# Kernel optimization log

Measured on AMD Instinct MI355X. Metric: run time of the kernel, lower is better.

The kernel has to match this reference:

```python
import jax, jax.numpy as jnp
import numpy as np

D_MODEL = 1024


def setup_inputs() -> dict:
    key = jax.random.key(0)
    k1, k2, k3 = jax.random.split(key, 3)
    x = jax.random.normal(k1, (4, 2048, D_MODEL), dtype=jnp.float32)
    w_qkv = jax.random.normal(k2, (D_MODEL, 3 * D_MODEL), dtype=jnp.float32) * (D_MODEL ** -0.5)
    b_qkv = jnp.zeros((3 * D_MODEL,), dtype=jnp.float32)
    w_out = jax.random.normal(k3, (D_MODEL, D_MODEL), dtype=jnp.float32) * (D_MODEL ** -0.5)
    b_out = jnp.zeros((D_MODEL,), dtype=jnp.float32)
    return {"x": x, "w_qkv": w_qkv, "b_qkv": b_qkv, "w_out": w_out, "b_out": b_out}


def reference(x, w_qkv, b_qkv, w_out, b_out):
    # x: [B, S, D]
    d_model = x.shape[-1]
    scale = jnp.asarray(d_model, x.dtype) ** 0.5
    qkv = x @ w_qkv + b_qkv                      # [B, S, 3D]
    q, k, v = jnp.split(qkv, 3, axis=-1)          # each [B, S, D]
    scores = jnp.einsum('bsd,btd->bst', q, k) / scale  # [B, S, S]
    attn = jax.nn.softmax(scores, axis=-1)
    out = jnp.einsum('bst,btd->bsd', attn, v)     # [B, S, D]
    return out @ w_out + b_out
```

## Files before the change

### kernel.cpp

```cpp
#include <hip/hip_runtime.h>
#include <hip/hip_bf16.h>
#include <cstdint>

typedef __attribute__((ext_vector_type(8))) short bf16x8;
typedef __attribute__((ext_vector_type(4))) float f32x4;
using bf16 = __hip_bfloat16;

static __device__ __forceinline__ float tofloat(float x) { return x; }
static __device__ __forceinline__ float tofloat(bf16 x) { return __bfloat162float(x); }
static __device__ __forceinline__ void storeval(float* p, float v) { *p = v; }
static __device__ __forceinline__ void storeval(bf16* p, float v) { *p = __float2bfloat16(v); }

#define MFMA_BF16 __builtin_amdgcn_mfma_f32_16x16x32_bf16

template <int N>
static __device__ __forceinline__ void vm_wait() {
    if constexpr (N == 0) asm volatile("s_waitcnt vmcnt(0)" ::: "memory");
    else if constexpr (N == 6) asm volatile("s_waitcnt vmcnt(6)" ::: "memory");
    else if constexpr (N == 8) asm volatile("s_waitcnt vmcnt(8)" ::: "memory");
}
static __device__ __forceinline__ void lgkm0() {
    asm volatile("s_waitcnt lgkmcnt(0)" ::: "memory");
    __builtin_amdgcn_sched_barrier(0);
}
static __device__ __forceinline__ void bar() { __builtin_amdgcn_s_barrier(); }
static __device__ __forceinline__ void vmem_fence() { __builtin_amdgcn_sched_barrier(0x38F); }
static __device__ __forceinline__ void gl_lds(const bf16* src, char* dst) {
    __builtin_amdgcn_global_load_lds((const __attribute__((address_space(1))) unsigned int*)src,
                                     (__attribute__((address_space(3))) unsigned int*)dst, 16, 0, 0);
}

__global__ __launch_bounds__(256) void convert_f32_bf16(const float* __restrict__ in,
                                                        bf16* __restrict__ out, long n) {
    long i = ((long)blockIdx.x * blockDim.x + threadIdx.x) * 8;
    if (i >= n) return;
    float4 a = *(const float4*)(in + i);
    float4 b = *(const float4*)(in + i + 4);
    bf16 t[8];
    t[0] = __float2bfloat16(a.x); t[1] = __float2bfloat16(a.y);
    t[2] = __float2bfloat16(a.z); t[3] = __float2bfloat16(a.w);
    t[4] = __float2bfloat16(b.x); t[5] = __float2bfloat16(b.y);
    t[6] = __float2bfloat16(b.z); t[7] = __float2bfloat16(b.w);
    *(uint4*)(out + i) = *(const uint4*)t;
}

template <typename SrcT>
__global__ __launch_bounds__(256) void transpose_to_bf16(const SrcT* __restrict__ src, long srcStride,
                                                         long srcBatch, bf16* __restrict__ dst,
                                                         long dstStride, long dstBatch) {
    __shared__ float tile[32][33];
    const SrcT* s = src + (long)blockIdx.z * srcBatch;
    bf16* d = dst + (long)blockIdx.z * dstBatch;
    long r0 = (long)blockIdx.y * 32, c0 = (long)blockIdx.x * 32;
    for (int i = threadIdx.y; i < 32; i += 8)
        tile[i][threadIdx.x] = tofloat(s[(r0 + i) * srcStride + c0 + threadIdx.x]);
    __syncthreads();
    for (int i = threadIdx.y; i < 32; i += 8)
        d[(c0 + i) * dstStride + r0 + threadIdx.x] = __float2bfloat16(tile[threadIdx.x][i]);
}

template <typename OutT, bool BIAS, int BM>
__global__ __launch_bounds__(512, 2) void gemm8p(
    const bf16* __restrict__ Ag, long lda, long batchA,
    const bf16* __restrict__ Bg, long ldb, long batchB,
    OutT* __restrict__ Cg, long ldc, long batchC,
    const float* __restrict__ bias, int K, float alpha, int nx, int ny) {
    constexpr int MR = BM / 32;
    constexpr int LA = BM / 128;
    constexpr int PA = BM * 64;
    constexpr int PB = 16384;
    constexpr int WV = 4 + 2 * LA;
    extern __shared__ __align__(16) char smem[];

    const int tid = threadIdx.x;
    const int wave = tid >> 6, lane = tid & 63, l16 = lane & 15, lhi = lane >> 4;
    const int wm = wave >> 2, wn = wave & 3;

    const int nwg = gridDim.x;
    const int l = (blockIdx.x & 7) * (nwg >> 3) + (blockIdx.x >> 3);
    const int pt = nx * ny;
    const int z = l / pt, rr = l % pt;
    const long mtile = (long)(rr / nx) * BM;
    const long ntile = (long)(rr % nx) * 256;

    const bf16* A = Ag + (long)z * batchA;
    const bf16* B = Bg + (long)z * batchB;
    OutT* C = Cg + (long)z * batchC;

    const int rp0 = tid >> 3;
    const int g8 = ((tid & 7) ^ ((tid >> 4) & 7)) * 8;
    const bf16* pA = A + (mtile + rp0) * lda + g8;
    const bf16* pB = B + (ntile + rp0) * ldb + g8;
    const int wb = wave * 1024;

    auto stageB = [&](int par, int t) {
        const bf16* s0 = pB + (long)t * 64;
        char* d0 = smem + 4 * PA + par * PB + wb;
        gl_lds(s0, d0);
        gl_lds(s0 + 64 * ldb, d0 + 8192);
        const bf16* s1 = s0 + 128 * ldb;
        char* d1 = smem + 4 * PA + 2 * PB + par * PB + wb;
        gl_lds(s1, d1);
        gl_lds(s1 + 64 * ldb, d1 + 8192);
    };
    auto stageA = [&](int par, int t) {
        const bf16* s0 = pA + (long)t * 64;
        char* d0 = smem + par * PA + wb;
        gl_lds(s0, d0);
        if constexpr (LA == 2) gl_lds(s0 + 64 * lda, d0 + 8192);
        const bf16* s1 = s0 + (long)(BM / 2) * lda;
        char* d1 = smem + 2 * PA + par * PA + wb;
        gl_lds(s1, d1);
        if constexpr (LA == 2) gl_lds(s1 + 64 * lda, d1 + 8192);
    };

    const int swz = (l16 >> 1) & 7;
    const int cb0 = (lhi ^ swz) * 16;
    const int cb1 = ((4 + lhi) ^ swz) * 16;
    const char* aBase = smem + wm * 2 * PA + l16 * 128;
    const char* bBase = smem + 4 * PA + (wn >> 1) * 2 * PB + ((wn & 1) * 64 + l16) * 128;

    bf16x8 aq[MR], bq[8];
    f32x4 acc[MR][4];
#pragma unroll
    for (int m = 0; m < MR; ++m)
#pragma unroll
        for (int n = 0; n < 4; ++n) acc[m][n] = f32x4{0.f, 0.f, 0.f, 0.f};

#define LDA_(par, h)                                                           \
    do {                                                                       \
        const char* p_ = aBase + (par) * PA + (h) * (PA / 2);                  \
        _Pragma("unroll")                                                      \
        for (int m_ = 0; m_ < MR / 2; ++m_) {                                  \
            aq[2 * m_]     = *(const bf16x8*)(p_ + m_ * 2048 + cb0);           \
            aq[2 * m_ + 1] = *(const bf16x8*)(p_ + m_ * 2048 + cb1);           \
        }                                                                      \
    } while (0)

#define LDB_(par, nlo)                                                         \
    do {                                                                       \
        const char* p_ = bBase + (par) * PB + (nlo) * 2048;                    \
        bq[(nlo) * 2 + 0] = *(const bf16x8*)(p_ + cb0);                        \
        bq[(nlo) * 2 + 1] = *(const bf16x8*)(p_ + cb1);                        \
        bq[(nlo) * 2 + 2] = *(const bf16x8*)(p_ + 2048 + cb0);                 \
        bq[(nlo) * 2 + 3] = *(const bf16x8*)(p_ + 2048 + cb1);                 \
    } while (0)

#define QUAD_(h, nlo)                                                          \
    do {                                                                       \
        __builtin_amdgcn_s_setprio(1);                                         \
        _Pragma("unroll")                                                      \
        for (int m_ = 0; m_ < MR / 2; ++m_) {                                  \
            acc[(h) * (MR / 2) + m_][(nlo) + 0] =                              \
                MFMA_BF16(aq[2 * m_], bq[(nlo) * 2 + 0], acc[(h) * (MR / 2) + m_][(nlo) + 0], 0, 0, 0); \
            acc[(h) * (MR / 2) + m_][(nlo) + 1] =                              \
                MFMA_BF16(aq[2 * m_], bq[(nlo) * 2 + 2], acc[(h) * (MR / 2) + m_][(nlo) + 1], 0, 0, 0); \
        }                                                                      \
        _Pragma("unroll")                                                      \
        for (int m_ = 0; m_ < MR / 2; ++m_) {                                  \
            acc[(h) * (MR / 2) + m_][(nlo) + 0] =                              \
                MFMA_BF16(aq[2 * m_ + 1], bq[(nlo) * 2 + 1], acc[(h) * (MR / 2) + m_][(nlo) + 0], 0, 0, 0); \
            acc[(h) * (MR / 2) + m_][(nlo) + 1] =                              \
                MFMA_BF16(aq[2 * m_ + 1], bq[(nlo) * 2 + 3], acc[(h) * (MR / 2) + m_][(nlo) + 1], 0, 0, 0); \
        }                                                                      \
        __builtin_amdgcn_s_setprio(0);                                         \
    } while (0)

#define KTILE(par, tstage, MODE)                                               \
    do {                                                                       \
                                                                       \
        LDA_(par, 0); LDB_(par, 0);                                            \
        bar(); lgkm0();                                                        \
        QUAD_(0, 0);                                                           \
        bar();                                                                 \
                                                                       \
        LDB_(par, 2);                                                          \
        bar(); lgkm0();                                                        \
        QUAD_(0, 2);                                                           \
        bar(); vmem_fence();                                                   \
            \
        LDA_(par, 1);                                                          \
        if (MODE == 0) stageB(par, tstage);                                    \
        bar(); lgkm0();                                                        \
        QUAD_(1, 2);                                                           \
        bar(); vmem_fence();                                                   \
                             \
        if (MODE == 0) stageA(par, tstage);                                    \
        QUAD_(1, 0);                                                           \
        if (MODE == 0) vm_wait<WV>();                                          \
        if (MODE == 1) vm_wait<0>();                                           \
        bar();                                                                 \
    } while (0)

    const int NT = K / 64;

    stageB(0, 0); stageA(0, 0);
    stageB(1, 1); stageA(1, 1);
    vm_wait<WV>();
    bar();

    for (int t = 0; t < NT - 2; ++t) KTILE(t & 1, t + 2, 0);
    KTILE(0, 0, 1);
    KTILE(1, 0, 2);

#pragma unroll
    for (int n = 0; n < 4; ++n) {
        long col = ntile + wn * 64 + n * 16 + l16;
        float bv = BIAS ? bias[col] : 0.0f;
#pragma unroll
        for (int am = 0; am < MR; ++am) {
            const int h_ = am / (MR / 2), mm = am % (MR / 2);
            long row = mtile + wm * (BM / 2) + h_ * (BM / 4) + mm * 16 + lhi * 4;
#pragma unroll
            for (int r2 = 0; r2 < 4; ++r2)
                storeval(&C[(row + r2) * ldc + col], acc[am][n][r2] * alpha + bv);
        }
    }
#undef KTILE
#undef QUAD_
#undef LDB_
#undef LDA_
}

__global__ __launch_bounds__(256) void softmax_rows_bf16(bf16* __restrict__ S, int ncols) {
    __shared__ float red[8];
    const long row = blockIdx.x;
    bf16* srow = S + row * ncols;
    const int tid = threadIdx.x;
    uint4 raw = *(const uint4*)(srow + tid * 8);
    const bf16* rb = (const bf16*)&raw;
    float v[8];
#pragma unroll
    for (int j = 0; j < 8; ++j) v[j] = __bfloat162float(rb[j]);
    float m = -3.4e38f;
#pragma unroll
    for (int j = 0; j < 8; ++j) m = fmaxf(m, v[j]);
#pragma unroll
    for (int off = 32; off; off >>= 1) m = fmaxf(m, __shfl_xor(m, off));
    if ((tid & 63) == 0) red[tid >> 6] = m;
    __syncthreads();
    m = fmaxf(fmaxf(red[0], red[1]), fmaxf(red[2], red[3]));
    float s = 0.0f;
#pragma unroll
    for (int j = 0; j < 8; ++j) {
        v[j] = __expf(v[j] - m);
        s += v[j];
    }
#pragma unroll
    for (int off = 32; off; off >>= 1) s += __shfl_xor(s, off);
    if ((tid & 63) == 0) red[4 + (tid >> 6)] = s;
    __syncthreads();
    s = red[4] + red[5] + red[6] + red[7];
    float inv = 1.0f / s;
    bf16 o[8];
#pragma unroll
    for (int j = 0; j < 8; ++j) o[j] = __float2bfloat16(v[j] * inv);
    *(uint4*)(srow + tid * 8) = *(const uint4*)o;
}

extern "C" void kernel_launch(void* const* d_in, const int* in_sizes, int n_in, void* d_out,
                              int out_size, void* d_ws, size_t ws_size, hipStream_t stream) {
    (void)in_sizes; (void)n_in; (void)out_size; (void)ws_size;
    const float* x = (const float*)d_in[0];
    const float* w_qkv = (const float*)d_in[1];
    const float* b_qkv = (const float*)d_in[2];
    const float* w_out = (const float*)d_in[3];
    const float* b_out = (const float*)d_in[4];
    float* out = (float*)d_out;

    const int B = 4, S = 2048, D = 1024;

    {
        (void)hipFuncSetAttribute((const void*)&gemm8p<bf16, true, 128>,
                                  hipFuncAttributeMaxDynamicSharedMemorySize, 98304);
        (void)hipFuncSetAttribute((const void*)&gemm8p<bf16, false, 256>,
                                  hipFuncAttributeMaxDynamicSharedMemorySize, 131072);
        (void)hipFuncSetAttribute((const void*)&gemm8p<bf16, false, 128>,
                                  hipFuncAttributeMaxDynamicSharedMemorySize, 98304);
        (void)hipFuncSetAttribute((const void*)&gemm8p<float, true, 128>,
                                  hipFuncAttributeMaxDynamicSharedMemorySize, 98304);
    }

    char* ws = (char*)d_ws;
    size_t off = 0;
    auto alloc = [&](size_t bytes) {
        char* p = ws + off;
        off += (bytes + 255) & ~(size_t)255;
        return p;
    };
    bf16* xb = (bf16*)alloc((size_t)B * S * D * 2);
    bf16* qkv = (bf16*)alloc((size_t)B * S * 3 * D * 2);
    bf16* wqkvT = (bf16*)alloc((size_t)3 * D * D * 2);
    bf16* woutT = (bf16*)alloc((size_t)D * D * 2);
    bf16* vt = (bf16*)alloc((size_t)B * D * S * 2);
    bf16* ao = (bf16*)alloc((size_t)B * S * D * 2);
    bf16* sc = (bf16*)alloc((size_t)B * S * S * 2);

    long nx_ = (long)B * S * D;
    convert_f32_bf16<<<(int)(nx_ / 8 / 256), 256, 0, stream>>>(x, xb, nx_);

    dim3 tb(32, 8);
    transpose_to_bf16<float><<<dim3(3 * D / 32, D / 32, 1), tb, 0, stream>>>(
        w_qkv, 3 * D, 0, wqkvT, D, 0);
    transpose_to_bf16<float><<<dim3(D / 32, D / 32, 1), tb, 0, stream>>>(
        w_out, D, 0, woutT, D, 0);

    gemm8p<bf16, true, 128><<<768, 512, 98304, stream>>>(
        xb, D, 0, wqkvT, D, 0, qkv, 3 * D, 0, b_qkv, D, 1.0f, 3 * D / 256, B * S / 128);

    transpose_to_bf16<bf16><<<dim3(D / 32, S / 32, B), tb, 0, stream>>>(
        qkv + 2 * D, 3 * D, (long)S * 3 * D, vt, S, (long)D * S);

    gemm8p<bf16, false, 256><<<256, 512, 131072, stream>>>(
        qkv, 3 * D, (long)S * 3 * D, qkv + D, 3 * D, (long)S * 3 * D,
        sc, S, (long)S * S, nullptr, D, 0.03125f, S / 256, S / 256);

    softmax_rows_bf16<<<B * S, 256, 0, stream>>>(sc, S);

    gemm8p<bf16, false, 128><<<256, 512, 98304, stream>>>(
        sc, S, (long)S * S, vt, S, (long)D * S,
        ao, D, (long)S * D, nullptr, S, 1.0f, D / 256, S / 128);

    gemm8p<float, true, 128><<<256, 512, 98304, stream>>>(
        ao, D, 0, woutT, D, 0, out, D, 0, b_out, D, 1.0f, D / 256, B * S / 128);
}
```

Measured before the change: 212.2 us.

## Software-pipeline LDS fragment reads across MFMA quads in GEMM kernel

Rewrites the GEMM main loop so LDS fragment reads for the next quad (and the next k-tile's first A/B fragments) are issued right after each MFMA quad, using double-buffered A register sets, instead of waiting on lgkmcnt before every quad. The kernel is specialized to a 128-row tile, and the scores GEMM now uses 128x256 tiles with 512 blocks instead of 256x256 with 256 blocks. Launch bounds drop to one block per CU, likely to allow more registers. The aim is to hide LDS latency behind MFMA work, at the cost of higher register pressure, lower occupancy, and a more fragile barrier/wait ordering.

```diff
diff --git a/kernel.cpp b/kernel.cpp
--- a/kernel.cpp
+++ b/kernel.cpp
@@ -17,14 +17,9 @@
 static __device__ __forceinline__ void vm_wait() {
     if constexpr (N == 0) asm volatile("s_waitcnt vmcnt(0)" ::: "memory");
     else if constexpr (N == 6) asm volatile("s_waitcnt vmcnt(6)" ::: "memory");
-    else if constexpr (N == 8) asm volatile("s_waitcnt vmcnt(8)" ::: "memory");
-}
-static __device__ __forceinline__ void lgkm0() {
-    asm volatile("s_waitcnt lgkmcnt(0)" ::: "memory");
-    __builtin_amdgcn_sched_barrier(0);
 }
 static __device__ __forceinline__ void bar() { __builtin_amdgcn_s_barrier(); }
-static __device__ __forceinline__ void vmem_fence() { __builtin_amdgcn_sched_barrier(0x38F); }
+static __device__ __forceinline__ void sb() { __builtin_amdgcn_sched_barrier(0xF); }
 static __device__ __forceinline__ void gl_lds(const bf16* src, char* dst) {
     __builtin_amdgcn_global_load_lds((const __attribute__((address_space(1))) unsigned int*)src,
                                      (__attribute__((address_space(3))) unsigned int*)dst, 16, 0, 0);
@@ -59,17 +54,14 @@
         d[(c0 + i) * dstStride + r0 + threadIdx.x] = __float2bfloat16(tile[threadIdx.x][i]);
 }
 
-template <typename OutT, bool BIAS, int BM>
-__global__ __launch_bounds__(512, 2) void gemm8p(
+template <typename OutT, bool BIAS>
+__global__ __launch_bounds__(512, 1) void gemm_sp(
     const bf16* __restrict__ Ag, long lda, long batchA,
     const bf16* __restrict__ Bg, long ldb, long batchB,
     OutT* __restrict__ Cg, long ldc, long batchC,
     const float* __restrict__ bias, int K, float alpha, int nx, int ny) {
-    constexpr int MR = BM / 32;
-    constexpr int LA = BM / 128;
-    constexpr int PA = BM * 64;
+    constexpr int PA = 8192;
     constexpr int PB = 16384;
-    constexpr int WV = 4 + 2 * LA;
     extern __shared__ __align__(16) char smem[];
 
     const int tid = threadIdx.x;
@@ -80,7 +72,7 @@
     const int l = (blockIdx.x & 7) * (nwg >> 3) + (blockIdx.x >> 3);
     const int pt = nx * ny;
     const int z = l / pt, rr = l % pt;
-    const long mtile = (long)(rr / nx) * BM;
+    const long mtile = (long)(rr / nx) * 128;
     const long ntile = (long)(rr % nx) * 256;
 
     const bf16* A = Ag + (long)z * batchA;
@@ -95,49 +87,43 @@
 
     auto stageB = [&](int par, int t) {
         const bf16* s0 = pB + (long)t * 64;
-        char* d0 = smem + 4 * PA + par * PB + wb;
+        char* d0 = smem + 32768 + par * PB + wb;
         gl_lds(s0, d0);
         gl_lds(s0 + 64 * ldb, d0 + 8192);
         const bf16* s1 = s0 + 128 * ldb;
-        char* d1 = smem + 4 * PA + 2 * PB + par * PB + wb;
+        char* d1 = smem + 32768 + 2 * PB + par * PB + wb;
         gl_lds(s1, d1);
         gl_lds(s1 + 64 * ldb, d1 + 8192);
     };
     auto stageA = [&](int par, int t) {
         const bf16* s0 = pA + (long)t * 64;
-        char* d0 = smem + par * PA + wb;
-        gl_lds(s0, d0);
-        if constexpr (LA == 2) gl_lds(s0 + 64 * lda, d0 + 8192);
-        const bf16* s1 = s0 + (long)(BM / 2) * lda;
-        char* d1 = smem + 2 * PA + par * PA + wb;
-        gl_lds(s1, d1);
-        if constexpr (LA == 2) gl_lds(s1 + 64 * lda, d1 + 8192);
+        gl_lds(s0, smem + par * PA + wb);
+        gl_lds(s0 + 64 * lda, smem + 2 * PA + par * PA + wb);
     };
 
     const int swz = (l16 >> 1) & 7;
     const int cb0 = (lhi ^ swz) * 16;
     const int cb1 = ((4 + lhi) ^ swz) * 16;
     const char* aBase = smem + wm * 2 * PA + l16 * 128;
-    const char* bBase = smem + 4 * PA + (wn >> 1) * 2 * PB + ((wn & 1) * 64 + l16) * 128;
-
-    bf16x8 aq[MR], bq[8];
-    f32x4 acc[MR][4];
-#pragma unroll
-    for (int m = 0; m < MR; ++m)
+    const char* bBase = smem + 32768 + (wn >> 1) * 2 * PB + ((wn & 1) * 64 + l16) * 128;
+
+    bf16x8 aqA[4], aqB[4], bq[8];
+    f32x4 acc[4][4];
+#pragma unroll
+    for (int m = 0; m < 4; ++m)
 #pragma unroll
         for (int n = 0; n < 4; ++n) acc[m][n] = f32x4{0.f, 0.f, 0.f, 0.f};
 
-#define LDA_(par, h)                                                           \
+#define RD_A(AQ, par, h)                                                       \
     do {                                                                       \
-        const char* p_ = aBase + (par) * PA + (h) * (PA / 2);                  \
-        _Pragma("unroll")                                                      \
-        for (int m_ = 0; m_ < MR / 2; ++m_) {                                  \
-            aq[2 * m_]     = *(const bf16x8*)(p_ + m_ * 2048 + cb0);           \
-            aq[2 * m_ + 1] = *(const bf16x8*)(p_ + m_ * 2048 + cb1);           \
-        }                                                                      \
+        const char* p_ = aBase + (par) * PA + (h) * 4096;                      \
+        AQ[0] = *(const bf16x8*)(p_ + cb0);                                    \
+        AQ[1] = *(const bf16x8*)(p_ + cb1);                                    \
+        AQ[2] = *(const bf16x8*)(p_ + 2048 + cb0);                             \
+        AQ[3] = *(const bf16x8*)(p_ + 2048 + cb1);                             \
     } while (0)
 
-#define LDB_(par, nlo)                                                         \
+#define RD_B(par, nlo)                                                         \
     do {                                                                       \
         const char* p_ = bBase + (par) * PB + (nlo) * 2048;                    \
         bq[(nlo) * 2 + 0] = *(const bf16x8*)(p_ + cb0);                        \
@@ -146,80 +132,79 @@
         bq[(nlo) * 2 + 3] = *(const bf16x8*)(p_ + 2048 + cb1);                 \
     } while (0)
 
-#define QUAD_(h, nlo)                                                          \
+#define QUAD_(AQ, h, nlo)                                                      \
     do {                                                                       \
         __builtin_amdgcn_s_setprio(1);                                         \
         _Pragma("unroll")                                                      \
-        for (int m_ = 0; m_ < MR / 2; ++m_) {                                  \
-            acc[(h) * (MR / 2) + m_][(nlo) + 0] =                              \
-                MFMA_BF16(aq[2 * m_], bq[(nlo) * 2 + 0], acc[(h) * (MR / 2) + m_][(nlo) + 0], 0, 0, 0); \
-            acc[(h) * (MR / 2) + m_][(nlo) + 1] =                              \
-                MFMA_BF16(aq[2 * m_], bq[(nlo) * 2 + 2], acc[(h) * (MR / 2) + m_][(nlo) + 1], 0, 0, 0); \
+        for (int m_ = 0; m_ < 2; ++m_) {                                       \
+            acc[(h)*2 + m_][(nlo) + 0] =                                       \
+                MFMA_BF16(AQ[2*m_], bq[(nlo)*2 + 0], acc[(h)*2 + m_][(nlo) + 0], 0, 0, 0); \
+            acc[(h)*2 + m_][(nlo) + 1] =                                       \
+                MFMA_BF16(AQ[2*m_], bq[(nlo)*2 + 2], acc[(h)*2 + m_][(nlo) + 1], 0, 0, 0); \
         }                                                                      \
         _Pragma("unroll")                                                      \
-        for (int m_ = 0; m_ < MR / 2; ++m_) {                                  \
-            acc[(h) * (MR / 2) + m_][(nlo) + 0] =                              \
-                MFMA_BF16(aq[2 * m_ + 1], bq[(nlo) * 2 + 1], acc[(h) * (MR / 2) + m_][(nlo) + 0], 0, 0, 0); \
-            acc[(h) * (MR / 2) + m_][(nlo) + 1] =                              \
-                MFMA_BF16(aq[2 * m_ + 1], bq[(nlo) * 2 + 3], acc[(h) * (MR / 2) + m_][(nlo) + 1], 0, 0, 0); \
+        for (int m_ = 0; m_ < 2; ++m_) {                                       \
+            acc[(h)*2 + m_][(nlo) + 0] =                                       \
+                MFMA_BF16(AQ[2*m_ + 1], bq[(nlo)*2 + 1], acc[(h)*2 + m_][(nlo) + 0], 0, 0, 0); \
+            acc[(h)*2 + m_][(nlo) + 1] =                                       \
+                MFMA_BF16(AQ[2*m_ + 1], bq[(nlo)*2 + 3], acc[(h)*2 + m_][(nlo) + 1], 0, 0, 0); \
         }                                                                      \
         __builtin_amdgcn_s_setprio(0);                                         \
     } while (0)
 
-#define KTILE(par, tstage, MODE)                                               \
+#define KT(par, tstage, MODE)                                                  \
     do {                                                                       \
-                                                                       \
-        LDA_(par, 0); LDB_(par, 0);                                            \
-        bar(); lgkm0();                                                        \
-        QUAD_(0, 0);                                                           \
-        bar();                                                                 \
-                                                                       \
-        LDB_(par, 2);                                                          \
-        bar(); lgkm0();                                                        \
-        QUAD_(0, 2);                                                           \
-        bar(); vmem_fence();                                                   \
-            \
-        LDA_(par, 1);                                                          \
+                                                    \
+        bar(); sb();                                                           \
+        QUAD_(aqA, 0, 0);                                                      \
+        RD_B(par, 2);                                                          \
+                                                    \
+        bar(); sb();                                                           \
+        QUAD_(aqA, 0, 2);                                                      \
+        RD_A(aqB, par, 1);                                                     \
+        vm_wait<0>();        \
+                               \
+        bar(); sb();             \
+        QUAD_(aqB, 1, 2);                                                      \
+        if (MODE < 2) RD_A(aqA, (par) ^ 1, 0);                                 \
         if (MODE == 0) stageB(par, tstage);                                    \
-        bar(); lgkm0();                                                        \
-        QUAD_(1, 2);                                                           \
-        bar(); vmem_fence();                                                   \
-                             \
+          \
+        bar(); sb();                                                           \
+        QUAD_(aqB, 1, 0);                                                      \
+        if (MODE < 2) RD_B((par) ^ 1, 0);                                      \
         if (MODE == 0) stageA(par, tstage);                                    \
-        QUAD_(1, 0);                                                           \
-        if (MODE == 0) vm_wait<WV>();                                          \
-        if (MODE == 1) vm_wait<0>();                                           \
-        bar();                                                                 \
     } while (0)
 
     const int NT = K / 64;
 
     stageB(0, 0); stageA(0, 0);
     stageB(1, 1); stageA(1, 1);
-    vm_wait<WV>();
-    bar();
-
-    for (int t = 0; t < NT - 2; ++t) KTILE(t & 1, t + 2, 0);
-    KTILE(0, 0, 1);
-    KTILE(1, 0, 2);
+    vm_wait<6>();
+    bar(); sb();
+    RD_A(aqA, 0, 0);
+    RD_B(0, 0);
+
+    for (int t = 0; t < NT - 2; ++t) KT(t & 1, t + 2, 0);
+    KT(0, 0, 1);
+    KT(1, 0, 2);
 
 #pragma unroll
     for (int n = 0; n < 4; ++n) {
         long col = ntile + wn * 64 + n * 16 + l16;
         float bv = BIAS ? bias[col] : 0.0f;
 #pragma unroll
-        for (int am = 0; am < MR; ++am) {
-            const int h_ = am / (MR / 2), mm = am % (MR / 2);
-            long row = mtile + wm * (BM / 2) + h_ * (BM / 4) + mm * 16 + lhi * 4;
+        for (int am = 0; am < 4; ++am) {
+            const int h_ = am >> 1, mm = am & 1;
+            long row = mtile + wm * 64 + h_ * 32 + mm * 16 + lhi * 4;
 #pragma unroll
             for (int r2 = 0; r2 < 4; ++r2)
                 storeval(&C[(row + r2) * ldc + col], acc[am][n][r2] * alpha + bv);
         }
     }
-#undef KTILE
+#undef KT
 #undef QUAD_
-#undef LDB_
-#undef LDA_
+#undef RD_B
+#undef RD_A
 }
 
 __global__ __launch_bounds__(256) void softmax_rows_bf16(bf16* __restrict__ S, int ncols) {
@@ -271,13 +256,11 @@
     const int B = 4, S = 2048, D = 1024;
 
     {
-        (void)hipFuncSetAttribute((const void*)&gemm8p<bf16, true, 128>,
+        (void)hipFuncSetAttribute((const void*)&gemm_sp<bf16, true>,
                                   hipFuncAttributeMaxDynamicSharedMemorySize, 98304);
-        (void)hipFuncSetAttribute((const void*)&gemm8p<bf16, false, 256>,
-                                  hipFuncAttributeMaxDynamicSharedMemorySize, 131072);
-        (void)hipFuncSetAttribute((const void*)&gemm8p<bf16, false, 128>,
+        (void)hipFuncSetAttribute((const void*)&gemm_sp<bf16, false>,
                                   hipFuncAttributeMaxDynamicSharedMemorySize, 98304);
-        (void)hipFuncSetAttribute((const void*)&gemm8p<float, true, 128>,
+        (void)hipFuncSetAttribute((const void*)&gemm_sp<float, true>,
                                   hipFuncAttributeMaxDynamicSharedMemorySize, 98304);
     }
 
@@ -305,22 +288,22 @@
     transpose_to_bf16<float><<<dim3(D / 32, D / 32, 1), tb, 0, stream>>>(
         w_out, D, 0, woutT, D, 0);
 
-    gemm8p<bf16, true, 128><<<768, 512, 98304, stream>>>(
+    gemm_sp<bf16, true><<<768, 512, 98304, stream>>>(
         xb, D, 0, wqkvT, D, 0, qkv, 3 * D, 0, b_qkv, D, 1.0f, 3 * D / 256, B * S / 128);
 
     transpose_to_bf16<bf16><<<dim3(D / 32, S / 32, B), tb, 0, stream>>>(
         qkv + 2 * D, 3 * D, (long)S * 3 * D, vt, S, (long)D * S);
 
-    gemm8p<bf16, false, 256><<<256, 512, 131072, stream>>>(
+    gemm_sp<bf16, false><<<512, 512, 98304, stream>>>(
         qkv, 3 * D, (long)S * 3 * D, qkv + D, 3 * D, (long)S * 3 * D,
-        sc, S, (long)S * S, nullptr, D, 0.03125f, S / 256, S / 256);
+        sc, S, (long)S * S, nullptr, D, 0.03125f, S / 256, S / 128);
 
     softmax_rows_bf16<<<B * S, 256, 0, stream>>>(sc, S);
 
-    gemm8p<bf16, false, 128><<<256, 512, 98304, stream>>>(
+    gemm_sp<bf16, false><<<256, 512, 98304, stream>>>(
         sc, S, (long)S * S, vt, S, (long)D * S,
         ao, D, (long)S * D, nullptr, S, 1.0f, D / 256, S / 128);
 
-    gemm8p<float, true, 128><<<256, 512, 98304, stream>>>(
+    gemm_sp<float, true><<<256, 512, 98304, stream>>>(
         ao, D, 0, woutT, D, 0, out, D, 0, b_out, D, 1.0f, D / 256, B * S / 128);
 }
```

Result: faster. 206.3 us (-2.8%).
